# Kernel tuning notes

Hardware: AMD Instinct MI355X
Metric: run time of the kernel (lower is better)

The kernel has to match this reference:

```python
import jax, jax.numpy as jnp
import numpy as np

SCALE_FACTOR = 4.0
DROPOUT_P = 0.5
DROPOUT_KEY = jax.random.key(42)  # fixed key: torch dropout is stochastic; we fix RNG for reproducibility


def setup_inputs() -> dict:
    key = jax.random.key(0)
    k1, k2 = jax.random.split(key)
    x1 = jax.random.normal(k1, (4096, 1024), dtype=jnp.float32)
    x2 = jax.random.normal(k2, (4096, 1024), dtype=jnp.float32)
    return {"x1": x1, "x2": x2}


def reference(x1, x2):
    # scores: [M, N] = x1 @ x2^T, scaled
    scores = jnp.matmul(x1, x2.T) * SCALE_FACTOR
    # F.softmax with no dim on 2-D input -> softmax over dim 1 (keys)
    attn = jax.nn.softmax(scores, axis=-1)
    # dropout p=0.5, train mode (inverted dropout: scale kept units by 1/(1-p))
    keep = jax.random.bernoulli(DROPOUT_KEY, 1.0 - DROPOUT_P, attn.shape)
    attn = jnp.where(keep, attn / (1.0 - DROPOUT_P), 0.0).astype(attn.dtype)
    # output: [M, D] = attn @ x2 (x2 reused as values)
    return jnp.matmul(attn, x2)
```

## Files before the change

### kernel.cpp

```cpp
#include <hip/hip_runtime.h>

typedef unsigned short u16;
typedef unsigned int   u32;
typedef __attribute__((ext_vector_type(4))) float f32x4;
typedef __attribute__((ext_vector_type(8))) short bf16x8;
typedef __attribute__((ext_vector_type(8))) unsigned short u16x8;
typedef __attribute__((ext_vector_type(4))) unsigned short u16x4;

#define MROWS 4096
#define DDIM  1024

__device__ __forceinline__ u16 f2bf(float f) {
  u32 u = __float_as_uint(f);
  return (u16)((u + 0x7FFFu + ((u >> 16) & 1u)) >> 16);
}
__device__ __forceinline__ float bf2f(u16 h) { return __uint_as_float(((u32)h) << 16); }

__global__ __launch_bounds__(256)
void expand3(const float4* __restrict__ x, u16* __restrict__ out, float scale, int patA) {
  int t = blockIdx.x * 256 + threadIdx.x;
  float4 v0 = x[(size_t)t * 2], v1 = x[(size_t)t * 2 + 1];
  float vv[8] = {v0.x*scale, v0.y*scale, v0.z*scale, v0.w*scale,
                 v1.x*scale, v1.y*scale, v1.z*scale, v1.w*scale};
  u16 o[24];
#pragma unroll
  for (int j = 0; j < 8; ++j) {
    u16 h = f2bf(vv[j]);
    u16 l = f2bf(vv[j] - bf2f(h));
    if (patA) { o[3*j]=h; o[3*j+1]=h; o[3*j+2]=l; }
    else      { o[3*j]=h; o[3*j+1]=l; o[3*j+2]=h; }
  }
  u16x8* dst = (u16x8*)(out + (size_t)t * 24);
#pragma unroll
  for (int q = 0; q < 3; ++q) {
    u16x8 w;
#pragma unroll
    for (int j = 0; j < 8; ++j) w[j] = o[q*8+j];
    dst[q] = w;
  }
}

__global__ __launch_bounds__(256)
void transpose_bf16(const float* __restrict__ x2, u16* __restrict__ VT) {
  __shared__ float tile[64][65];
  int tid = threadIdx.x;
  int dt = blockIdx.x;
  int kt = blockIdx.y;
#pragma unroll
  for (int it = 0; it < 16; ++it) {
    int lin = it * 256 + tid;
    int r = lin >> 6, c = lin & 63;
    tile[r][c] = x2[(size_t)(kt*64 + r) * DDIM + dt*64 + c];
  }
  __syncthreads();
#pragma unroll
  for (int it = 0; it < 16; ++it) {
    int lin = it * 256 + tid;
    int dr = lin >> 6, kc = lin & 63;
    VT[(size_t)(dt*64 + dr) * MROWS + kt*64 + kc] = f2bf(tile[kc][dr]);
  }
}

__device__ __forceinline__ void gload16(const u16* g, u16* l) {
  __builtin_amdgcn_global_load_lds(
      (const __attribute__((address_space(1))) void*)g,
      (__attribute__((address_space(3))) void*)l, 16, 0, 0);
}

#define BARRIER() do { asm volatile("" ::: "memory"); __builtin_amdgcn_s_barrier(); \
                       asm volatile("" ::: "memory"); } while (0)
#define LGKM0()   do { asm volatile("s_waitcnt lgkmcnt(0)" ::: "memory"); \
                       __builtin_amdgcn_sched_barrier(0); } while (0)
#define VMCNT6()  do { asm volatile("s_waitcnt vmcnt(6)" ::: "memory"); } while (0)

__device__ __forceinline__ void read_a4(bf16x8 (&aF)[4][2], const u16* base, const int (&off)[4][2]) {
#pragma unroll
  for (int m = 0; m < 4; ++m)
#pragma unroll
    for (int kx = 0; kx < 2; ++kx)
      aF[m][kx] = *(const bf16x8*)(base + off[m][kx]);
}
__device__ __forceinline__ void read_b2(bf16x8 (&bF)[2][2], const u16* base, const int (&off)[2][2]) {
#pragma unroll
  for (int n = 0; n < 2; ++n)
#pragma unroll
    for (int kx = 0; kx < 2; ++kx)
      bF[n][kx] = *(const bf16x8*)(base + off[n][kx]);
}
__device__ __forceinline__ void mma_quad(f32x4 (&acc)[8][4], const bf16x8 (&aF)[4][2],
                                         const bf16x8 (&bF)[2][2], int MH, int NH) {
#pragma unroll
  for (int kx = 0; kx < 2; ++kx)
#pragma unroll
    for (int m = 0; m < 4; ++m)
#pragma unroll
      for (int n = 0; n < 2; ++n)
        acc[MH*4+m][NH*2+n] = __builtin_amdgcn_mfma_f32_16x16x32_bf16(
            aF[m][kx], bF[n][kx], acc[MH*4+m][NH*2+n], 0, 0, 0);
}

__global__ __launch_bounds__(512, 2)
void gemm256(const u16* __restrict__ A, const u16* __restrict__ Bt, float* __restrict__ C,
             int M, int N, int K, int ntpc) {
  __shared__ u16 smem[65536];
  const int tid = threadIdx.x;
  const int lane = tid & 63;
  const int w = tid >> 6;
  const int wr = w >> 2;
  const int wc = w & 3;
  const int fr = lane & 15;
  const int hi = lane >> 4;

  const long bm = (long)blockIdx.y * 256;
  const long bn = (long)blockIdx.x * 256;
  const size_t kcol0 = (size_t)blockIdx.z * ntpc * 64;
  float* Cz = C + (size_t)blockIdx.z * (size_t)M * N;

  const int srow = tid >> 3;
  const int scol = (((tid & 7) ^ (srow & 7)) << 3);
  const u16* Abase = A + (size_t)(bm + srow) * K + kcol0 + scol;
  const u16* Bbase = Bt + (size_t)(bn + srow) * K + kcol0 + scol;

  int offA[4][2], offB[2][2];
#pragma unroll
  for (int m = 0; m < 4; ++m)
#pragma unroll
    for (int kx = 0; kx < 2; ++kx) {
      int r = m*32 + wr*16 + fr;
      int c0 = kx*4 + hi;
      offA[m][kx] = r*64 + (((c0 ^ (r & 7))) << 3);
    }
#pragma unroll
  for (int n = 0; n < 2; ++n)
#pragma unroll
    for (int kx = 0; kx < 2; ++kx) {
      int r = n*64 + wc*16 + fr;
      int c0 = kx*4 + hi;
      offB[n][kx] = r*64 + (((c0 ^ (r & 7))) << 3);
    }

  f32x4 acc[8][4];
#pragma unroll
  for (int m = 0; m < 8; ++m)
#pragma unroll
    for (int n = 0; n < 4; ++n) acc[m][n] = (f32x4){0.f, 0.f, 0.f, 0.f};
  bf16x8 aF[4][2], b0F[2][2], b1F[2][2];

#define STAGE_A(TAU,H,D) do { \
    const u16* _s = Abase + (size_t)(H)*128*K + (size_t)(TAU)*64; \
    u16* _d = smem + ((D)*2+(H))*8192 + tid*8; \
    gload16(_s, _d); gload16(_s + (size_t)64*K, _d + 4096); } while (0)
#define STAGE_B(TAU,H,D) do { \
    const u16* _s = Bbase + (size_t)(H)*128*K + (size_t)(TAU)*64; \
    u16* _d = smem + 32768 + ((D)*2+(H))*8192 + tid*8; \
    gload16(_s, _d); gload16(_s + (size_t)64*K, _d + 4096); } while (0)

  STAGE_A(0,0,0); STAGE_B(0,0,0); STAGE_B(0,1,0); STAGE_A(0,1,0);
  STAGE_A(1,0,1); STAGE_B(1,0,1); STAGE_B(1,1,1);
  VMCNT6();
  BARRIER();

  const int nt = ntpc;
  for (int T = 0; T < nt; T += 2) {
    const int t1 = T + 1;
    const int t2 = (T + 2 < nt) ? T + 2 : nt - 1;
    const int t3 = (T + 3 < nt) ? T + 3 : nt - 1;

    read_a4(aF, smem + 0, offA);
    read_b2(b0F, smem + 32768, offB);
    STAGE_A(t1, 1, 1);
    BARRIER(); LGKM0();
    __builtin_amdgcn_s_setprio(1); mma_quad(acc, aF, b0F, 0, 0); __builtin_amdgcn_s_setprio(0);
    BARRIER();
    read_b2(b1F, smem + 40960, offB);
    STAGE_A(t2, 0, 0);
    BARRIER(); LGKM0();
    __builtin_amdgcn_s_setprio(1); mma_quad(acc, aF, b1F, 0, 1); __builtin_amdgcn_s_setprio(0);
    BARRIER();
    read_a4(aF, smem + 8192, offA);
    STAGE_B(t2, 0, 0);
    BARRIER(); LGKM0();
    __builtin_amdgcn_s_setprio(1); mma_quad(acc, aF, b0F, 1, 0); __builtin_amdgcn_s_setprio(0);
    BARRIER();
    STAGE_B(t2, 1, 0);
    VMCNT6();
    BARRIER(); LGKM0();
    __builtin_amdgcn_s_setprio(1); mma_quad(acc, aF, b1F, 1, 1); __builtin_amdgcn_s_setprio(0);
    BARRIER();
    read_a4(aF, smem + 16384, offA);
    read_b2(b0F, smem + 49152, offB);
    STAGE_A(t2, 1, 0);
    BARRIER(); LGKM0();
    __builtin_amdgcn_s_setprio(1); mma_quad(acc, aF, b0F, 0, 0); __builtin_amdgcn_s_setprio(0);
    BARRIER();
    read_b2(b1F, smem + 57344, offB);
    STAGE_A(t3, 0, 1);
    BARRIER(); LGKM0();
    __builtin_amdgcn_s_setprio(1); mma_quad(acc, aF, b1F, 0, 1); __builtin_amdgcn_s_setprio(0);
    BARRIER();
    read_a4(aF, smem + 24576, offA);
    STAGE_B(t3, 0, 1);
    BARRIER(); LGKM0();
    __builtin_amdgcn_s_setprio(1); mma_quad(acc, aF, b0F, 1, 0); __builtin_amdgcn_s_setprio(0);
    BARRIER();
    STAGE_B(t3, 1, 1);
    VMCNT6();
    BARRIER(); LGKM0();
    __builtin_amdgcn_s_setprio(1); mma_quad(acc, aF, b1F, 1, 1); __builtin_amdgcn_s_setprio(0);
    BARRIER();
  }
#undef STAGE_A
#undef STAGE_B

#pragma unroll
  for (int m = 0; m < 8; ++m)
#pragma unroll
    for (int n = 0; n < 4; ++n) {
      size_t row0 = (size_t)(bm + m*32 + wr*16 + hi*4);
      size_t col  = (size_t)(bn + n*64 + wc*16 + fr);
#pragma unroll
      for (int r = 0; r < 4; ++r)
        Cz[(row0 + r) * N + col] = acc[m][n][r];
    }
}

__device__ __forceinline__ u32 rotl32(u32 x, int r) { return (x << r) | (x >> (32 - r)); }

__device__ __forceinline__ u32 threefry_bits(u32 n) {
  const u32 K0 = 0u, K1 = 42u, K2 = 0x1BD11BDAu ^ 0u ^ 42u;
  u32 x0 = K0;
  u32 x1 = n + K1;
#define TF4(a,b,c,d) \
  x0 += x1; x1 = rotl32(x1, a); x1 ^= x0; \
  x0 += x1; x1 = rotl32(x1, b); x1 ^= x0; \
  x0 += x1; x1 = rotl32(x1, c); x1 ^= x0; \
  x0 += x1; x1 = rotl32(x1, d); x1 ^= x0;
  TF4(13,15,26,6);  x0 += K1; x1 += K2 + 1u;
  TF4(17,29,16,24); x0 += K2; x1 += K0 + 2u;
  TF4(13,15,26,6);  x0 += K0; x1 += K1 + 3u;
  TF4(17,29,16,24); x0 += K1; x1 += K2 + 4u;
  TF4(13,15,26,6);  x0 += K2; x1 += K0 + 5u;
#undef TF4
  return x0 ^ x1;
}

__global__ __launch_bounds__(256)
void softmax_dropout(const float* __restrict__ S, u16* __restrict__ P) {
  const int tid  = threadIdx.x;
  const int lane = tid & 63;
  const int w    = tid >> 6;
  const int row  = blockIdx.x * 4 + w;
  const float4* Sr = (const float4*)(S + (size_t)row * MROWS);
  float4 v[16];
#pragma unroll
  for (int i = 0; i < 16; ++i) v[i] = Sr[i * 64 + lane];
  float m = -3.0e38f;
#pragma unroll
  for (int i = 0; i < 16; ++i)
    m = fmaxf(m, fmaxf(fmaxf(v[i].x, v[i].y), fmaxf(v[i].z, v[i].w)));
#pragma unroll
  for (int off = 32; off > 0; off >>= 1) m = fmaxf(m, __shfl_xor(m, off, 64));
  float s = 0.0f;
#pragma unroll
  for (int i = 0; i < 16; ++i) {
    v[i].x = __expf(v[i].x - m); v[i].y = __expf(v[i].y - m);
    v[i].z = __expf(v[i].z - m); v[i].w = __expf(v[i].w - m);
    s += v[i].x + v[i].y + v[i].z + v[i].w;
  }
#pragma unroll
  for (int off = 32; off > 0; off >>= 1) s += __shfl_xor(s, off, 64);
  const float inv = 2.0f / s;
  u16* Pr = P + (size_t)row * MROWS;
#pragma unroll
  for (int i = 0; i < 16; ++i) {
    int j0 = (i * 64 + lane) * 4;
    u32 base = (u32)row * 4096u + (u32)j0;
    float e[4] = {v[i].x, v[i].y, v[i].z, v[i].w};
    u16x4 o;
#pragma unroll
    for (int c = 0; c < 4; ++c) {
      u32 bits = threefry_bits(base + (u32)c);
      float val = (bits & 0x80000000u) ? 0.0f : e[c] * inv;
      o[c] = f2bf(val);
    }
    *(u16x4*)(Pr + j0) = o;
  }
}

__global__ __launch_bounds__(256)
void reduce4(const float4* __restrict__ p, float4* __restrict__ out) {
  size_t i = (size_t)blockIdx.x * 256 + threadIdx.x;
  const size_t NP = (size_t)MROWS * DDIM / 4;
  float4 a = p[i], b = p[i + NP], c = p[i + 2*NP], d = p[i + 3*NP];
  float4 r;
  r.x = a.x + b.x + c.x + d.x;
  r.y = a.y + b.y + c.y + d.y;
  r.z = a.z + b.z + c.z + d.z;
  r.w = a.w + b.w + c.w + d.w;
  out[i] = r;
}

extern "C" void kernel_launch(void* const* d_in, const int* in_sizes, int n_in,
                              void* d_out, int out_size, void* d_ws, size_t ws_size,
                              hipStream_t stream) {
  const float* x1 = (const float*)d_in[0];
  const float* x2 = (const float*)d_in[1];
  float* out = (float*)d_out;
  char* ws = (char*)d_ws;

  const size_t OFF_XB = 25165824;
  const size_t OFF_VT = 50331648;
  const size_t OFF_S  = 58720256;
  const size_t NEED   = 125829120;
  if (ws_size < NEED) {
    hipMemsetAsync(d_out, 0x7F, (size_t)out_size * sizeof(float), stream);
    return;
  }
  u16*   XA = (u16*)(ws);
  u16*   XB = (u16*)(ws + OFF_XB);
  u16*   VT = (u16*)(ws + OFF_VT);
  float* S  = (float*)(ws + OFF_S);
  float* PT = (float*)(ws + OFF_S);
  u16*   P  = (u16*)(ws);

  expand3<<<2048, 256, 0, stream>>>((const float4*)x1, XA, 4.0f, 1);
  expand3<<<2048, 256, 0, stream>>>((const float4*)x2, XB, 1.0f, 0);
  transpose_bf16<<<dim3(16, 64), 256, 0, stream>>>(x2, VT);
  gemm256<<<dim3(16, 16, 1), 512, 0, stream>>>(XA, XB, S, 4096, 4096, 3072, 48);
  softmax_dropout<<<1024, 256, 0, stream>>>(S, P);
  gemm256<<<dim3(4, 16, 4), 512, 0, stream>>>(P, VT, PT, 4096, 1024, 4096, 16);
  reduce4<<<4096, 256, 0, stream>>>((const float4*)PT, (float4*)out);
}
```

Measured before the change: 199.0 us.

## Precompute dropout bitmask in expand kernels and restructure GEMM LDS reads with block swizzle

Threefry dropout bits move out of softmax into the expand3 kernels, which pack them into a 2 MB bitmask that softmax reads back as words. The GEMM inner loop is reorganised into two 4x4 accumulator halves with even/odd k-fragment reads and grouped staging. A block-index remap spreads neighbouring tiles apart for better cache locality. The intent is to shorten the compute-heavy softmax pass and tighten the GEMM schedule, at the cost of extra mask memory traffic and more work in the expand kernels.

New measurement: 205.5 us. 3.2% more time.

```diff
diff --git a/kernel.cpp b/kernel.cpp
--- a/kernel.cpp
+++ b/kernel.cpp
@@ -16,216 +16,7 @@
 }
 __device__ __forceinline__ float bf2f(u16 h) { return __uint_as_float(((u32)h) << 16); }
 
-__global__ __launch_bounds__(256)
-void expand3(const float4* __restrict__ x, u16* __restrict__ out, float scale, int patA) {
-  int t = blockIdx.x * 256 + threadIdx.x;
-  float4 v0 = x[(size_t)t * 2], v1 = x[(size_t)t * 2 + 1];
-  float vv[8] = {v0.x*scale, v0.y*scale, v0.z*scale, v0.w*scale,
-                 v1.x*scale, v1.y*scale, v1.z*scale, v1.w*scale};
-  u16 o[24];
-#pragma unroll
-  for (int j = 0; j < 8; ++j) {
-    u16 h = f2bf(vv[j]);
-    u16 l = f2bf(vv[j] - bf2f(h));
-    if (patA) { o[3*j]=h; o[3*j+1]=h; o[3*j+2]=l; }
-    else      { o[3*j]=h; o[3*j+1]=l; o[3*j+2]=h; }
-  }
-  u16x8* dst = (u16x8*)(out + (size_t)t * 24);
-#pragma unroll
-  for (int q = 0; q < 3; ++q) {
-    u16x8 w;
-#pragma unroll
-    for (int j = 0; j < 8; ++j) w[j] = o[q*8+j];
-    dst[q] = w;
-  }
-}
-
-__global__ __launch_bounds__(256)
-void transpose_bf16(const float* __restrict__ x2, u16* __restrict__ VT) {
-  __shared__ float tile[64][65];
-  int tid = threadIdx.x;
-  int dt = blockIdx.x;
-  int kt = blockIdx.y;
-#pragma unroll
-  for (int it = 0; it < 16; ++it) {
-    int lin = it * 256 + tid;
-    int r = lin >> 6, c = lin & 63;
-    tile[r][c] = x2[(size_t)(kt*64 + r) * DDIM + dt*64 + c];
-  }
-  __syncthreads();
-#pragma unroll
-  for (int it = 0; it < 16; ++it) {
-    int lin = it * 256 + tid;
-    int dr = lin >> 6, kc = lin & 63;
-    VT[(size_t)(dt*64 + dr) * MROWS + kt*64 + kc] = f2bf(tile[kc][dr]);
-  }
-}
-
-__device__ __forceinline__ void gload16(const u16* g, u16* l) {
-  __builtin_amdgcn_global_load_lds(
-      (const __attribute__((address_space(1))) void*)g,
-      (__attribute__((address_space(3))) void*)l, 16, 0, 0);
-}
-
-#define BARRIER() do { asm volatile("" ::: "memory"); __builtin_amdgcn_s_barrier(); \
-                       asm volatile("" ::: "memory"); } while (0)
-#define LGKM0()   do { asm volatile("s_waitcnt lgkmcnt(0)" ::: "memory"); \
-                       __builtin_amdgcn_sched_barrier(0); } while (0)
-#define VMCNT6()  do { asm volatile("s_waitcnt vmcnt(6)" ::: "memory"); } while (0)
-
-__device__ __forceinline__ void read_a4(bf16x8 (&aF)[4][2], const u16* base, const int (&off)[4][2]) {
-#pragma unroll
-  for (int m = 0; m < 4; ++m)
-#pragma unroll
-    for (int kx = 0; kx < 2; ++kx)
-      aF[m][kx] = *(const bf16x8*)(base + off[m][kx]);
-}
-__device__ __forceinline__ void read_b2(bf16x8 (&bF)[2][2], const u16* base, const int (&off)[2][2]) {
-#pragma unroll
-  for (int n = 0; n < 2; ++n)
-#pragma unroll
-    for (int kx = 0; kx < 2; ++kx)
-      bF[n][kx] = *(const bf16x8*)(base + off[n][kx]);
-}
-__device__ __forceinline__ void mma_quad(f32x4 (&acc)[8][4], const bf16x8 (&aF)[4][2],
-                                         const bf16x8 (&bF)[2][2], int MH, int NH) {
-#pragma unroll
-  for (int kx = 0; kx < 2; ++kx)
-#pragma unroll
-    for (int m = 0; m < 4; ++m)
-#pragma unroll
-      for (int n = 0; n < 2; ++n)
-        acc[MH*4+m][NH*2+n] = __builtin_amdgcn_mfma_f32_16x16x32_bf16(
-            aF[m][kx], bF[n][kx], acc[MH*4+m][NH*2+n], 0, 0, 0);
-}
-
-__global__ __launch_bounds__(512, 2)
-void gemm256(const u16* __restrict__ A, const u16* __restrict__ Bt, float* __restrict__ C,
-             int M, int N, int K, int ntpc) {
-  __shared__ u16 smem[65536];
-  const int tid = threadIdx.x;
-  const int lane = tid & 63;
-  const int w = tid >> 6;
-  const int wr = w >> 2;
-  const int wc = w & 3;
-  const int fr = lane & 15;
-  const int hi = lane >> 4;
-
-  const long bm = (long)blockIdx.y * 256;
-  const long bn = (long)blockIdx.x * 256;
-  const size_t kcol0 = (size_t)blockIdx.z * ntpc * 64;
-  float* Cz = C + (size_t)blockIdx.z * (size_t)M * N;
-
-  const int srow = tid >> 3;
-  const int scol = (((tid & 7) ^ (srow & 7)) << 3);
-  const u16* Abase = A + (size_t)(bm + srow) * K + kcol0 + scol;
-  const u16* Bbase = Bt + (size_t)(bn + srow) * K + kcol0 + scol;
-
-  int offA[4][2], offB[2][2];
-#pragma unroll
-  for (int m = 0; m < 4; ++m)
-#pragma unroll
-    for (int kx = 0; kx < 2; ++kx) {
-      int r = m*32 + wr*16 + fr;
-      int c0 = kx*4 + hi;
-      offA[m][kx] = r*64 + (((c0 ^ (r & 7))) << 3);
-    }
-#pragma unroll
-  for (int n = 0; n < 2; ++n)
-#pragma unroll
-    for (int kx = 0; kx < 2; ++kx) {
-      int r = n*64 + wc*16 + fr;
-      int c0 = kx*4 + hi;
-      offB[n][kx] = r*64 + (((c0 ^ (r & 7))) << 3);
-    }
-
-  f32x4 acc[8][4];
-#pragma unroll
-  for (int m = 0; m < 8; ++m)
-#pragma unroll
-    for (int n = 0; n < 4; ++n) acc[m][n] = (f32x4){0.f, 0.f, 0.f, 0.f};
-  bf16x8 aF[4][2], b0F[2][2], b1F[2][2];
-
-#define STAGE_A(TAU,H,D) do { \
-    const u16* _s = Abase + (size_t)(H)*128*K + (size_t)(TAU)*64; \
-    u16* _d = smem + ((D)*2+(H))*8192 + tid*8; \
-    gload16(_s, _d); gload16(_s + (size_t)64*K, _d + 4096); } while (0)
-#define STAGE_B(TAU,H,D) do { \
-    const u16* _s = Bbase + (size_t)(H)*128*K + (size_t)(TAU)*64; \
-    u16* _d = smem + 32768 + ((D)*2+(H))*8192 + tid*8; \
-    gload16(_s, _d); gload16(_s + (size_t)64*K, _d + 4096); } while (0)
-
-  STAGE_A(0,0,0); STAGE_B(0,0,0); STAGE_B(0,1,0); STAGE_A(0,1,0);
-  STAGE_A(1,0,1); STAGE_B(1,0,1); STAGE_B(1,1,1);
-  VMCNT6();
-  BARRIER();
-
-  const int nt = ntpc;
-  for (int T = 0; T < nt; T += 2) {
-    const int t1 = T + 1;
-    const int t2 = (T + 2 < nt) ? T + 2 : nt - 1;
-    const int t3 = (T + 3 < nt) ? T + 3 : nt - 1;
-
-    read_a4(aF, smem + 0, offA);
-    read_b2(b0F, smem + 32768, offB);
-    STAGE_A(t1, 1, 1);
-    BARRIER(); LGKM0();
-    __builtin_amdgcn_s_setprio(1); mma_quad(acc, aF, b0F, 0, 0); __builtin_amdgcn_s_setprio(0);
-    BARRIER();
-    read_b2(b1F, smem + 40960, offB);
-    STAGE_A(t2, 0, 0);
-    BARRIER(); LGKM0();
-    __builtin_amdgcn_s_setprio(1); mma_quad(acc, aF, b1F, 0, 1); __builtin_amdgcn_s_setprio(0);
-    BARRIER();
-    read_a4(aF, smem + 8192, offA);
-    STAGE_B(t2, 0, 0);
-    BARRIER(); LGKM0();
-    __builtin_amdgcn_s_setprio(1); mma_quad(acc, aF, b0F, 1, 0); __builtin_amdgcn_s_setprio(0);
-    BARRIER();
-    STAGE_B(t2, 1, 0);
-    VMCNT6();
-    BARRIER(); LGKM0();
-    __builtin_amdgcn_s_setprio(1); mma_quad(acc, aF, b1F, 1, 1); __builtin_amdgcn_s_setprio(0);
-    BARRIER();
-    read_a4(aF, smem + 16384, offA);
-    read_b2(b0F, smem + 49152, offB);
-    STAGE_A(t2, 1, 0);
-    BARRIER(); LGKM0();
-    __builtin_amdgcn_s_setprio(1); mma_quad(acc, aF, b0F, 0, 0); __builtin_amdgcn_s_setprio(0);
-    BARRIER();
-    read_b2(b1F, smem + 57344, offB);
-    STAGE_A(t3, 0, 1);
-    BARRIER(); LGKM0();
-    __builtin_amdgcn_s_setprio(1); mma_quad(acc, aF, b1F, 0, 1); __builtin_amdgcn_s_setprio(0);
-    BARRIER();
-    read_a4(aF, smem + 24576, offA);
-    STAGE_B(t3, 0, 1);
-    BARRIER(); LGKM0();
-    __builtin_amdgcn_s_setprio(1); mma_quad(acc, aF, b0F, 1, 0); __builtin_amdgcn_s_setprio(0);
-    BARRIER();
-    STAGE_B(t3, 1, 1);
-    VMCNT6();
-    BARRIER(); LGKM0();
-    __builtin_amdgcn_s_setprio(1); mma_quad(acc, aF, b1F, 1, 1); __builtin_amdgcn_s_setprio(0);
-    BARRIER();
-  }
-#undef STAGE_A
-#undef STAGE_B
-
-#pragma unroll
-  for (int m = 0; m < 8; ++m)
-#pragma unroll
-    for (int n = 0; n < 4; ++n) {
-      size_t row0 = (size_t)(bm + m*32 + wr*16 + hi*4);
-      size_t col  = (size_t)(bn + n*64 + wc*16 + fr);
-#pragma unroll
-      for (int r = 0; r < 4; ++r)
-        Cz[(row0 + r) * N + col] = acc[m][n][r];
-    }
-}
-
 __device__ __forceinline__ u32 rotl32(u32 x, int r) { return (x << r) | (x >> (32 - r)); }
-
 __device__ __forceinline__ u32 threefry_bits(u32 n) {
   const u32 K0 = 0u, K1 = 42u, K2 = 0x1BD11BDAu ^ 0u ^ 42u;
   u32 x0 = K0;
@@ -245,7 +36,223 @@
 }
 
 __global__ __launch_bounds__(256)
-void softmax_dropout(const float* __restrict__ S, u16* __restrict__ P) {
+void expand3(const float4* __restrict__ x, u16* __restrict__ out, float scale, int patA,
+             u32* __restrict__ mask, u32 wordBase, u32 nWords) {
+  int t = blockIdx.x * 256 + threadIdx.x;
+  float4 v0 = x[(size_t)t * 2], v1 = x[(size_t)t * 2 + 1];
+  float vv[8] = {v0.x*scale, v0.y*scale, v0.z*scale, v0.w*scale,
+                 v1.x*scale, v1.y*scale, v1.z*scale, v1.w*scale};
+  u16 o[24];
+#pragma unroll
+  for (int j = 0; j < 8; ++j) {
+    u16 h = f2bf(vv[j]);
+    u16 l = f2bf(vv[j] - bf2f(h));
+    if (patA) { o[3*j]=h; o[3*j+1]=h; o[3*j+2]=l; }
+    else      { o[3*j]=h; o[3*j+1]=l; o[3*j+2]=h; }
+  }
+  u16x8* dst = (u16x8*)(out + (size_t)t * 24);
+#pragma unroll
+  for (int q = 0; q < 3; ++q) {
+    u16x8 wv;
+#pragma unroll
+    for (int j = 0; j < 8; ++j) wv[j] = o[q*8+j];
+    dst[q] = wv;
+  }
+  if ((u32)t < nWords) {
+    u32 wi = wordBase + (u32)t;
+    u32 n0 = wi * 32u;
+    u32 wbits = 0;
+#pragma unroll 4
+    for (int b = 0; b < 32; ++b) wbits |= (threefry_bits(n0 + (u32)b) >> 31) << b;
+    mask[wi] = wbits;
+  }
+}
+
+__global__ __launch_bounds__(256)
+void transpose_bf16(const float* __restrict__ x2, u16* __restrict__ VT) {
+  __shared__ float tile[64][65];
+  int tid = threadIdx.x;
+  int dt = blockIdx.x;
+  int kt = blockIdx.y;
+#pragma unroll
+  for (int it = 0; it < 16; ++it) {
+    int lin = it * 256 + tid;
+    int r = lin >> 6, c = lin & 63;
+    tile[r][c] = x2[(size_t)(kt*64 + r) * DDIM + dt*64 + c];
+  }
+  __syncthreads();
+#pragma unroll
+  for (int it = 0; it < 16; ++it) {
+    int lin = it * 256 + tid;
+    int dr = lin >> 6, kc = lin & 63;
+    VT[(size_t)(dt*64 + dr) * MROWS + kt*64 + kc] = f2bf(tile[kc][dr]);
+  }
+}
+
+__device__ __forceinline__ void gload16(const u16* g, u16* l) {
+  __builtin_amdgcn_global_load_lds(
+      (const __attribute__((address_space(1))) void*)g,
+      (__attribute__((address_space(3))) void*)l, 16, 0, 0);
+}
+
+#define BARRIER() do { asm volatile("" ::: "memory"); __builtin_amdgcn_s_barrier(); \
+                       asm volatile("" ::: "memory"); } while (0)
+#define LGKM0()   do { asm volatile("s_waitcnt lgkmcnt(0)" ::: "memory"); \
+                       __builtin_amdgcn_sched_barrier(0); } while (0)
+#define VMCNT6()  do { asm volatile("s_waitcnt vmcnt(6)" ::: "memory"); } while (0)
+
+__device__ __forceinline__ void mma4x4(f32x4 (&accq)[4][4], const bf16x8 (&a)[4],
+                                       const bf16x8 (&b)[4]) {
+#pragma unroll
+  for (int m = 0; m < 4; ++m)
+#pragma unroll
+    for (int n = 0; n < 4; ++n)
+      accq[m][n] = __builtin_amdgcn_mfma_f32_16x16x32_bf16(a[m], b[n], accq[m][n], 0, 0, 0);
+}
+
+__global__ __launch_bounds__(512, 2)
+void gemm256(const u16* __restrict__ A, const u16* __restrict__ Bt, float* __restrict__ C,
+             int M, int N, int K, int ntpc) {
+  __shared__ u16 smem[65536];
+  const int tid = threadIdx.x;
+  const int lane = tid & 63;
+  const int w = tid >> 6;
+  const int wr = w >> 2;
+  const int wc = w & 3;
+  const int fr = lane & 15;
+  const int hi = lane >> 4;
+
+  const int nbxy = gridDim.x * gridDim.y;
+  const int id0 = blockIdx.y * gridDim.x + blockIdx.x;
+  const int id  = (id0 & 7) * (nbxy >> 3) + (id0 >> 3);
+  const int bxi = id % gridDim.x;
+  const int byi = id / gridDim.x;
+
+  const long bm = (long)byi * 256;
+  const long bn = (long)bxi * 256;
+  const size_t kcol0 = (size_t)blockIdx.z * ntpc * 64;
+  float* Cz = C + (size_t)blockIdx.z * (size_t)M * N;
+
+  const int srow = tid >> 3;
+  const int scol = (((tid & 7) ^ (srow & 7)) << 3);
+  const u16* Abase = A  + (size_t)(bm + srow) * K + kcol0 + scol;
+  const u16* Bbase = Bt + (size_t)(bn + srow) * K + kcol0 + scol;
+
+  const int csw0 = ((hi)     ^ (fr & 7)) << 3;
+  const int csw1 = ((4 + hi) ^ (fr & 7)) << 3;
+  const int arow = (wr*16 + fr) * 64;
+  const int brow = (wc*16 + fr) * 64;
+
+#define RD_A(dst, D, H, CSW) do { \
+    const u16* _b = smem + ((D)*2+(H))*8192 + arow + (CSW); \
+    dst[0] = *(const bf16x8*)(_b); \
+    dst[1] = *(const bf16x8*)(_b + 2048); \
+    dst[2] = *(const bf16x8*)(_b + 4096); \
+    dst[3] = *(const bf16x8*)(_b + 6144); } while (0)
+#define RD_B(dst, D, CSW) do { \
+    const u16* _b0 = smem + 32768 + ((D)*2+0)*8192 + brow + (CSW); \
+    const u16* _b1 = smem + 32768 + ((D)*2+1)*8192 + brow + (CSW); \
+    dst[0] = *(const bf16x8*)(_b0); \
+    dst[1] = *(const bf16x8*)(_b0 + 4096); \
+    dst[2] = *(const bf16x8*)(_b1); \
+    dst[3] = *(const bf16x8*)(_b1 + 4096); } while (0)
+
+  f32x4 accL[4][4], accH[4][4];
+#pragma unroll
+  for (int m = 0; m < 4; ++m)
+#pragma unroll
+    for (int n = 0; n < 4; ++n) {
+      accL[m][n] = (f32x4){0.f, 0.f, 0.f, 0.f};
+      accH[m][n] = (f32x4){0.f, 0.f, 0.f, 0.f};
+    }
+  bf16x8 aE[4], aO[4], bE[4], bO[4];
+
+#define STAGE_A(TAU,H,D) do { \
+    const u16* _s = Abase + (size_t)(H)*128*K + (size_t)(TAU)*64; \
+    u16* _d = smem + ((D)*2+(H))*8192 + tid*8; \
+    gload16(_s, _d); gload16(_s + (size_t)64*K, _d + 4096); } while (0)
+#define STAGE_B(TAU,H,D) do { \
+    const u16* _s = Bbase + (size_t)(H)*128*K + (size_t)(TAU)*64; \
+    u16* _d = smem + 32768 + ((D)*2+(H))*8192 + tid*8; \
+    gload16(_s, _d); gload16(_s + (size_t)64*K, _d + 4096); } while (0)
+
+  STAGE_A(0,0,0); STAGE_B(0,0,0); STAGE_B(0,1,0); STAGE_A(0,1,0);
+  STAGE_A(1,0,1); STAGE_B(1,0,1); STAGE_B(1,1,1);
+  VMCNT6();
+  BARRIER();
+
+  const int nt = ntpc;
+  for (int T = 0; T < nt; T += 2) {
+    const int t1 = T + 1;
+    const int t2 = (T + 2 < nt) ? T + 2 : nt - 1;
+    const int t3 = (T + 3 < nt) ? T + 3 : nt - 1;
+
+    RD_A(aE, 0, 0, csw0);
+    RD_B(bE, 0, csw0);
+    STAGE_A(t1, 1, 1);
+    BARRIER(); LGKM0();
+    __builtin_amdgcn_s_setprio(1); mma4x4(accL, aE, bE); __builtin_amdgcn_s_setprio(0);
+    BARRIER();
+    RD_A(aO, 0, 0, csw1);
+    RD_B(bO, 0, csw1);
+    BARRIER(); LGKM0();
+    __builtin_amdgcn_s_setprio(1); mma4x4(accL, aO, bO); __builtin_amdgcn_s_setprio(0);
+    BARRIER();
+    RD_A(aE, 0, 1, csw0);
+    STAGE_A(t2, 0, 0); STAGE_B(t2, 0, 0); STAGE_B(t2, 1, 0);
+    BARRIER(); LGKM0();
+    __builtin_amdgcn_s_setprio(1); mma4x4(accH, aE, bE); __builtin_amdgcn_s_setprio(0);
+    BARRIER();
+    RD_A(aO, 0, 1, csw1);
+    VMCNT6();
+    BARRIER(); LGKM0();
+    __builtin_amdgcn_s_setprio(1); mma4x4(accH, aO, bO); __builtin_amdgcn_s_setprio(0);
+    BARRIER();
+    RD_A(aE, 1, 0, csw0);
+    RD_B(bE, 1, csw0);
+    STAGE_A(t2, 1, 0);
+    BARRIER(); LGKM0();
+    __builtin_amdgcn_s_setprio(1); mma4x4(accL, aE, bE); __builtin_amdgcn_s_setprio(0);
+    BARRIER();
+    RD_A(aO, 1, 0, csw1);
+    RD_B(bO, 1, csw1);
+    BARRIER(); LGKM0();
+    __builtin_amdgcn_s_setprio(1); mma4x4(accL, aO, bO); __builtin_amdgcn_s_setprio(0);
+    BARRIER();
+    RD_A(aE, 1, 1, csw0);
+    STAGE_A(t3, 0, 1); STAGE_B(t3, 0, 1); STAGE_B(t3, 1, 1);
+    BARRIER(); LGKM0();
+    __builtin_amdgcn_s_setprio(1); mma4x4(accH, aE, bE); __builtin_amdgcn_s_setprio(0);
+    BARRIER();
+    RD_A(aO, 1, 1, csw1);
+    VMCNT6();
+    BARRIER(); LGKM0();
+    __builtin_amdgcn_s_setprio(1); mma4x4(accH, aO, bO); __builtin_amdgcn_s_setprio(0);
+    BARRIER();
+  }
+#undef STAGE_A
+#undef STAGE_B
+#undef RD_A
+#undef RD_B
+
+#pragma unroll
+  for (int m = 0; m < 4; ++m)
+#pragma unroll
+    for (int n = 0; n < 4; ++n) {
+      size_t rowL = (size_t)(bm + m*32 + wr*16 + hi*4);
+      size_t rowH = rowL + 128;
+      size_t col  = (size_t)(bn + n*64 + wc*16 + fr);
+#pragma unroll
+      for (int r = 0; r < 4; ++r) {
+        Cz[(rowL + r) * N + col] = accL[m][n][r];
+        Cz[(rowH + r) * N + col] = accH[m][n][r];
+      }
+    }
+}
+
+__global__ __launch_bounds__(256)
+void softmax_dropout(const float* __restrict__ S, const u32* __restrict__ mask,
+                     u16* __restrict__ P) {
   const int tid  = threadIdx.x;
   const int lane = tid & 63;
   const int w    = tid >> 6;
@@ -271,16 +278,17 @@
   for (int off = 32; off > 0; off >>= 1) s += __shfl_xor(s, off, 64);
   const float inv = 2.0f / s;
   u16* Pr = P + (size_t)row * MROWS;
+  const u32* Mw = mask + (size_t)row * 128;
 #pragma unroll
   for (int i = 0; i < 16; ++i) {
     int j0 = (i * 64 + lane) * 4;
-    u32 base = (u32)row * 4096u + (u32)j0;
+    u32 word = Mw[j0 >> 5];
+    int sh = j0 & 31;
     float e[4] = {v[i].x, v[i].y, v[i].z, v[i].w};
     u16x4 o;
 #pragma unroll
     for (int c = 0; c < 4; ++c) {
-      u32 bits = threefry_bits(base + (u32)c);
-      float val = (bits & 0x80000000u) ? 0.0f : e[c] * inv;
+      float val = ((word >> (sh + c)) & 1u) ? 0.0f : e[c] * inv;
       o[c] = f2bf(val);
     }
     *(u16x4*)(Pr + j0) = o;
@@ -308,10 +316,11 @@
   float* out = (float*)d_out;
   char* ws = (char*)d_ws;
 
-  const size_t OFF_XB = 25165824;
-  const size_t OFF_VT = 50331648;
-  const size_t OFF_S  = 58720256;
-  const size_t NEED   = 125829120;
+  const size_t OFF_XB   = 25165824;
+  const size_t OFF_VT   = 50331648;
+  const size_t OFF_S    = 58720256;
+  const size_t OFF_MASK = 125829120;
+  const size_t NEED     = 127926272;
   if (ws_size < NEED) {
     hipMemsetAsync(d_out, 0x7F, (size_t)out_size * sizeof(float), stream);
     return;
@@ -321,13 +330,14 @@
   u16*   VT = (u16*)(ws + OFF_VT);
   float* S  = (float*)(ws + OFF_S);
   float* PT = (float*)(ws + OFF_S);
+  u32*   MK = (u32*)(ws + OFF_MASK);
   u16*   P  = (u16*)(ws);
 
-  expand3<<<2048, 256, 0, stream>>>((const float4*)x1, XA, 4.0f, 1);
-  expand3<<<2048, 256, 0, stream>>>((const float4*)x2, XB, 1.0f, 0);
+  expand3<<<2048, 256, 0, stream>>>((const float4*)x1, XA, 4.0f, 1, MK, 0u, 262144u);
+  expand3<<<2048, 256, 0, stream>>>((const float4*)x2, XB, 1.0f, 0, MK, 262144u, 262144u);
   transpose_bf16<<<dim3(16, 64), 256, 0, stream>>>(x2, VT);
   gemm256<<<dim3(16, 16, 1), 512, 0, stream>>>(XA, XB, S, 4096, 4096, 3072, 48);
-  softmax_dropout<<<1024, 256, 0, stream>>>(S, P);
+  softmax_dropout<<<1024, 256, 0, stream>>>(S, MK, P);
   gemm256<<<dim3(4, 16, 4), 512, 0, stream>>>(P, VT, PT, 4096, 1024, 4096, 16);
   reduce4<<<4096, 256, 0, stream>>>((const float4*)PT, (float4*)out);
 }
```

## Compute dropout mask bits inside QK^T GEMM mainloop to hide RNG cost

Applied to the files above, without the earlier changes.

The threefry dropout bits are now generated inside the first GEMM's MFMA loop, interleaved between barriers, and packed into a bitmask in workspace. The softmax kernel reads these mask words instead of running threefry per element. The aim is to hide the integer-heavy RNG work under the MFMA-bound GEMM and make softmax memory-bound. The cost is extra VALU work and register pressure in the GEMM plus a small mask write and read.

After: 205.8 us. 1.03x slower.

```diff
diff --git a/kernel.cpp b/kernel.cpp
--- a/kernel.cpp
+++ b/kernel.cpp
@@ -16,216 +16,7 @@
 }
 __device__ __forceinline__ float bf2f(u16 h) { return __uint_as_float(((u32)h) << 16); }
 
-__global__ __launch_bounds__(256)
-void expand3(const float4* __restrict__ x, u16* __restrict__ out, float scale, int patA) {
-  int t = blockIdx.x * 256 + threadIdx.x;
-  float4 v0 = x[(size_t)t * 2], v1 = x[(size_t)t * 2 + 1];
-  float vv[8] = {v0.x*scale, v0.y*scale, v0.z*scale, v0.w*scale,
-                 v1.x*scale, v1.y*scale, v1.z*scale, v1.w*scale};
-  u16 o[24];
-#pragma unroll
-  for (int j = 0; j < 8; ++j) {
-    u16 h = f2bf(vv[j]);
-    u16 l = f2bf(vv[j] - bf2f(h));
-    if (patA) { o[3*j]=h; o[3*j+1]=h; o[3*j+2]=l; }
-    else      { o[3*j]=h; o[3*j+1]=l; o[3*j+2]=h; }
-  }
-  u16x8* dst = (u16x8*)(out + (size_t)t * 24);
-#pragma unroll
-  for (int q = 0; q < 3; ++q) {
-    u16x8 w;
-#pragma unroll
-    for (int j = 0; j < 8; ++j) w[j] = o[q*8+j];
-    dst[q] = w;
-  }
-}
-
-__global__ __launch_bounds__(256)
-void transpose_bf16(const float* __restrict__ x2, u16* __restrict__ VT) {
-  __shared__ float tile[64][65];
-  int tid = threadIdx.x;
-  int dt = blockIdx.x;
-  int kt = blockIdx.y;
-#pragma unroll
-  for (int it = 0; it < 16; ++it) {
-    int lin = it * 256 + tid;
-    int r = lin >> 6, c = lin & 63;
-    tile[r][c] = x2[(size_t)(kt*64 + r) * DDIM + dt*64 + c];
-  }
-  __syncthreads();
-#pragma unroll
-  for (int it = 0; it < 16; ++it) {
-    int lin = it * 256 + tid;
-    int dr = lin >> 6, kc = lin & 63;
-    VT[(size_t)(dt*64 + dr) * MROWS + kt*64 + kc] = f2bf(tile[kc][dr]);
-  }
-}
-
-__device__ __forceinline__ void gload16(const u16* g, u16* l) {
-  __builtin_amdgcn_global_load_lds(
-      (const __attribute__((address_space(1))) void*)g,
-      (__attribute__((address_space(3))) void*)l, 16, 0, 0);
-}
-
-#define BARRIER() do { asm volatile("" ::: "memory"); __builtin_amdgcn_s_barrier(); \
-                       asm volatile("" ::: "memory"); } while (0)
-#define LGKM0()   do { asm volatile("s_waitcnt lgkmcnt(0)" ::: "memory"); \
-                       __builtin_amdgcn_sched_barrier(0); } while (0)
-#define VMCNT6()  do { asm volatile("s_waitcnt vmcnt(6)" ::: "memory"); } while (0)
-
-__device__ __forceinline__ void read_a4(bf16x8 (&aF)[4][2], const u16* base, const int (&off)[4][2]) {
-#pragma unroll
-  for (int m = 0; m < 4; ++m)
-#pragma unroll
-    for (int kx = 0; kx < 2; ++kx)
-      aF[m][kx] = *(const bf16x8*)(base + off[m][kx]);
-}
-__device__ __forceinline__ void read_b2(bf16x8 (&bF)[2][2], const u16* base, const int (&off)[2][2]) {
-#pragma unroll
-  for (int n = 0; n < 2; ++n)
-#pragma unroll
-    for (int kx = 0; kx < 2; ++kx)
-      bF[n][kx] = *(const bf16x8*)(base + off[n][kx]);
-}
-__device__ __forceinline__ void mma_quad(f32x4 (&acc)[8][4], const bf16x8 (&aF)[4][2],
-                                         const bf16x8 (&bF)[2][2], int MH, int NH) {
-#pragma unroll
-  for (int kx = 0; kx < 2; ++kx)
-#pragma unroll
-    for (int m = 0; m < 4; ++m)
-#pragma unroll
-      for (int n = 0; n < 2; ++n)
-        acc[MH*4+m][NH*2+n] = __builtin_amdgcn_mfma_f32_16x16x32_bf16(
-            aF[m][kx], bF[n][kx], acc[MH*4+m][NH*2+n], 0, 0, 0);
-}
-
-__global__ __launch_bounds__(512, 2)
-void gemm256(const u16* __restrict__ A, const u16* __restrict__ Bt, float* __restrict__ C,
-             int M, int N, int K, int ntpc) {
-  __shared__ u16 smem[65536];
-  const int tid = threadIdx.x;
-  const int lane = tid & 63;
-  const int w = tid >> 6;
-  const int wr = w >> 2;
-  const int wc = w & 3;
-  const int fr = lane & 15;
-  const int hi = lane >> 4;
-
-  const long bm = (long)blockIdx.y * 256;
-  const long bn = (long)blockIdx.x * 256;
-  const size_t kcol0 = (size_t)blockIdx.z * ntpc * 64;
-  float* Cz = C + (size_t)blockIdx.z * (size_t)M * N;
-
-  const int srow = tid >> 3;
-  const int scol = (((tid & 7) ^ (srow & 7)) << 3);
-  const u16* Abase = A + (size_t)(bm + srow) * K + kcol0 + scol;
-  const u16* Bbase = Bt + (size_t)(bn + srow) * K + kcol0 + scol;
-
-  int offA[4][2], offB[2][2];
-#pragma unroll
-  for (int m = 0; m < 4; ++m)
-#pragma unroll
-    for (int kx = 0; kx < 2; ++kx) {
-      int r = m*32 + wr*16 + fr;
-      int c0 = kx*4 + hi;
-      offA[m][kx] = r*64 + (((c0 ^ (r & 7))) << 3);
-    }
-#pragma unroll
-  for (int n = 0; n < 2; ++n)
-#pragma unroll
-    for (int kx = 0; kx < 2; ++kx) {
-      int r = n*64 + wc*16 + fr;
-      int c0 = kx*4 + hi;
-      offB[n][kx] = r*64 + (((c0 ^ (r & 7))) << 3);
-    }
-
-  f32x4 acc[8][4];
-#pragma unroll
-  for (int m = 0; m < 8; ++m)
-#pragma unroll
-    for (int n = 0; n < 4; ++n) acc[m][n] = (f32x4){0.f, 0.f, 0.f, 0.f};
-  bf16x8 aF[4][2], b0F[2][2], b1F[2][2];
-
-#define STAGE_A(TAU,H,D) do { \
-    const u16* _s = Abase + (size_t)(H)*128*K + (size_t)(TAU)*64; \
-    u16* _d = smem + ((D)*2+(H))*8192 + tid*8; \
-    gload16(_s, _d); gload16(_s + (size_t)64*K, _d + 4096); } while (0)
-#define STAGE_B(TAU,H,D) do { \
-    const u16* _s = Bbase + (size_t)(H)*128*K + (size_t)(TAU)*64; \
-    u16* _d = smem + 32768 + ((D)*2+(H))*8192 + tid*8; \
-    gload16(_s, _d); gload16(_s + (size_t)64*K, _d + 4096); } while (0)
-
-  STAGE_A(0,0,0); STAGE_B(0,0,0); STAGE_B(0,1,0); STAGE_A(0,1,0);
-  STAGE_A(1,0,1); STAGE_B(1,0,1); STAGE_B(1,1,1);
-  VMCNT6();
-  BARRIER();
-
-  const int nt = ntpc;
-  for (int T = 0; T < nt; T += 2) {
-    const int t1 = T + 1;
-    const int t2 = (T + 2 < nt) ? T + 2 : nt - 1;
-    const int t3 = (T + 3 < nt) ? T + 3 : nt - 1;
-
-    read_a4(aF, smem + 0, offA);
-    read_b2(b0F, smem + 32768, offB);
-    STAGE_A(t1, 1, 1);
-    BARRIER(); LGKM0();
-    __builtin_amdgcn_s_setprio(1); mma_quad(acc, aF, b0F, 0, 0); __builtin_amdgcn_s_setprio(0);
-    BARRIER();
-    read_b2(b1F, smem + 40960, offB);
-    STAGE_A(t2, 0, 0);
-    BARRIER(); LGKM0();
-    __builtin_amdgcn_s_setprio(1); mma_quad(acc, aF, b1F, 0, 1); __builtin_amdgcn_s_setprio(0);
-    BARRIER();
-    read_a4(aF, smem + 8192, offA);
-    STAGE_B(t2, 0, 0);
-    BARRIER(); LGKM0();
-    __builtin_amdgcn_s_setprio(1); mma_quad(acc, aF, b0F, 1, 0); __builtin_amdgcn_s_setprio(0);
-    BARRIER();
-    STAGE_B(t2, 1, 0);
-    VMCNT6();
-    BARRIER(); LGKM0();
-    __builtin_amdgcn_s_setprio(1); mma_quad(acc, aF, b1F, 1, 1); __builtin_amdgcn_s_setprio(0);
-    BARRIER();
-    read_a4(aF, smem + 16384, offA);
-    read_b2(b0F, smem + 49152, offB);
-    STAGE_A(t2, 1, 0);
-    BARRIER(); LGKM0();
-    __builtin_amdgcn_s_setprio(1); mma_quad(acc, aF, b0F, 0, 0); __builtin_amdgcn_s_setprio(0);
-    BARRIER();
-    read_b2(b1F, smem + 57344, offB);
-    STAGE_A(t3, 0, 1);
-    BARRIER(); LGKM0();
-    __builtin_amdgcn_s_setprio(1); mma_quad(acc, aF, b1F, 0, 1); __builtin_amdgcn_s_setprio(0);
-    BARRIER();
-    read_a4(aF, smem + 24576, offA);
-    STAGE_B(t3, 0, 1);
-    BARRIER(); LGKM0();
-    __builtin_amdgcn_s_setprio(1); mma_quad(acc, aF, b0F, 1, 0); __builtin_amdgcn_s_setprio(0);
-    BARRIER();
-    STAGE_B(t3, 1, 1);
-    VMCNT6();
-    BARRIER(); LGKM0();
-    __builtin_amdgcn_s_setprio(1); mma_quad(acc, aF, b1F, 1, 1); __builtin_amdgcn_s_setprio(0);
-    BARRIER();
-  }
-#undef STAGE_A
-#undef STAGE_B
-
-#pragma unroll
-  for (int m = 0; m < 8; ++m)
-#pragma unroll
-    for (int n = 0; n < 4; ++n) {
-      size_t row0 = (size_t)(bm + m*32 + wr*16 + hi*4);
-      size_t col  = (size_t)(bn + n*64 + wc*16 + fr);
-#pragma unroll
-      for (int r = 0; r < 4; ++r)
-        Cz[(row0 + r) * N + col] = acc[m][n][r];
-    }
-}
-
 __device__ __forceinline__ u32 rotl32(u32 x, int r) { return (x << r) | (x >> (32 - r)); }
-
 __device__ __forceinline__ u32 threefry_bits(u32 n) {
   const u32 K0 = 0u, K1 = 42u, K2 = 0x1BD11BDAu ^ 0u ^ 42u;
   u32 x0 = K0;
@@ -245,7 +36,241 @@
 }
 
 __global__ __launch_bounds__(256)
-void softmax_dropout(const float* __restrict__ S, u16* __restrict__ P) {
+void expand3(const float4* __restrict__ x, u16* __restrict__ out, float scale, int patA) {
+  int t = blockIdx.x * 256 + threadIdx.x;
+  float4 v0 = x[(size_t)t * 2], v1 = x[(size_t)t * 2 + 1];
+  float vv[8] = {v0.x*scale, v0.y*scale, v0.z*scale, v0.w*scale,
+                 v1.x*scale, v1.y*scale, v1.z*scale, v1.w*scale};
+  u16 o[24];
+#pragma unroll
+  for (int j = 0; j < 8; ++j) {
+    u16 h = f2bf(vv[j]);
+    u16 l = f2bf(vv[j] - bf2f(h));
+    if (patA) { o[3*j]=h; o[3*j+1]=h; o[3*j+2]=l; }
+    else      { o[3*j]=h; o[3*j+1]=l; o[3*j+2]=h; }
+  }
+  u16x8* dst = (u16x8*)(out + (size_t)t * 24);
+#pragma unroll
+  for (int q = 0; q < 3; ++q) {
+    u16x8 wv;
+#pragma unroll
+    for (int j = 0; j < 8; ++j) wv[j] = o[q*8+j];
+    dst[q] = wv;
+  }
+}
+
+__global__ __launch_bounds__(256)
+void transpose_bf16(const float* __restrict__ x2, u16* __restrict__ VT) {
+  __shared__ float tile[64][65];
+  int tid = threadIdx.x;
+  int dt = blockIdx.x;
+  int kt = blockIdx.y;
+#pragma unroll
+  for (int it = 0; it < 16; ++it) {
+    int lin = it * 256 + tid;
+    int r = lin >> 6, c = lin & 63;
+    tile[r][c] = x2[(size_t)(kt*64 + r) * DDIM + dt*64 + c];
+  }
+  __syncthreads();
+#pragma unroll
+  for (int it = 0; it < 16; ++it) {
+    int lin = it * 256 + tid;
+    int dr = lin >> 6, kc = lin & 63;
+    VT[(size_t)(dt*64 + dr) * MROWS + kt*64 + kc] = f2bf(tile[kc][dr]);
+  }
+}
+
+__device__ __forceinline__ void gload16(const u16* g, u16* l) {
+  __builtin_amdgcn_global_load_lds(
+      (const __attribute__((address_space(1))) void*)g,
+      (__attribute__((address_space(3))) void*)l, 16, 0, 0);
+}
+
+#define BARRIER() do { asm volatile("" ::: "memory"); __builtin_amdgcn_s_barrier(); \
+                       asm volatile("" ::: "memory"); } while (0)
+#define LGKM0()   do { asm volatile("s_waitcnt lgkmcnt(0)" ::: "memory"); \
+                       __builtin_amdgcn_sched_barrier(0); } while (0)
+#define VMCNT6()  do { asm volatile("s_waitcnt vmcnt(6)" ::: "memory"); } while (0)
+
+__device__ __forceinline__ void read_a4(bf16x8 (&aF)[4][2], const u16* base, const int (&off)[4][2]) {
+#pragma unroll
+  for (int m = 0; m < 4; ++m)
+#pragma unroll
+    for (int kx = 0; kx < 2; ++kx)
+      aF[m][kx] = *(const bf16x8*)(base + off[m][kx]);
+}
+__device__ __forceinline__ void read_b2(bf16x8 (&bF)[2][2], const u16* base, const int (&off)[2][2]) {
+#pragma unroll
+  for (int n = 0; n < 2; ++n)
+#pragma unroll
+    for (int kx = 0; kx < 2; ++kx)
+      bF[n][kx] = *(const bf16x8*)(base + off[n][kx]);
+}
+__device__ __forceinline__ void mma_quad(f32x4 (&acc)[8][4], const bf16x8 (&aF)[4][2],
+                                         const bf16x8 (&bF)[2][2], int MH, int NH) {
+#pragma unroll
+  for (int kx = 0; kx < 2; ++kx)
+#pragma unroll
+    for (int m = 0; m < 4; ++m)
+#pragma unroll
+      for (int n = 0; n < 2; ++n)
+        acc[MH*4+m][NH*2+n] = __builtin_amdgcn_mfma_f32_16x16x32_bf16(
+            aF[m][kx], bF[n][kx], acc[MH*4+m][NH*2+n], 0, 0, 0);
+}
+
+template <bool DOMASK>
+__global__ __launch_bounds__(512, 2)
+void gemm256(const u16* __restrict__ A, const u16* __restrict__ Bt, float* __restrict__ C,
+             int M, int N, int K, int ntpc, u32* __restrict__ mask) {
+  __shared__ u16 smem[65536];
+  const int tid = threadIdx.x;
+  const int lane = tid & 63;
+  const int w = tid >> 6;
+  const int wr = w >> 2;
+  const int wc = w & 3;
+  const int fr = lane & 15;
+  const int hi = lane >> 4;
+
+  const long bm = (long)blockIdx.y * 256;
+  const long bn = (long)blockIdx.x * 256;
+  const size_t kcol0 = (size_t)blockIdx.z * ntpc * 64;
+  float* Cz = C + (size_t)blockIdx.z * (size_t)M * N;
+
+  const int srow = tid >> 3;
+  const int scol = (((tid & 7) ^ (srow & 7)) << 3);
+  const u16* Abase = A  + (size_t)(bm + srow) * K + kcol0 + scol;
+  const u16* Bbase = Bt + (size_t)(bn + srow) * K + kcol0 + scol;
+
+  int offA[4][2], offB[2][2];
+#pragma unroll
+  for (int m = 0; m < 4; ++m)
+#pragma unroll
+    for (int kx = 0; kx < 2; ++kx) {
+      int r = m*32 + wr*16 + fr;
+      int c0 = kx*4 + hi;
+      offA[m][kx] = r*64 + (((c0 ^ (r & 7))) << 3);
+    }
+#pragma unroll
+  for (int n = 0; n < 2; ++n)
+#pragma unroll
+    for (int kx = 0; kx < 2; ++kx) {
+      int r = n*64 + wc*16 + fr;
+      int c0 = kx*4 + hi;
+      offB[n][kx] = r*64 + (((c0 ^ (r & 7))) << 3);
+    }
+
+  f32x4 acc[8][4];
+#pragma unroll
+  for (int m = 0; m < 8; ++m)
+#pragma unroll
+    for (int n = 0; n < 4; ++n) acc[m][n] = (f32x4){0.f, 0.f, 0.f, 0.f};
+  bf16x8 aF[4][2], b0F[2][2], b1F[2][2];
+
+  u32 mw0 = 0, mw1 = 0, mw2 = 0, mw3 = 0;
+  u32 ci = 0;
+#define MASK_STEP() do { if (DOMASK) { if (ci < 128u) { \
+    u32 lw  = (u32)tid * 4u + (ci >> 5); \
+    u32 n   = (((u32)bm + (lw >> 3)) << 12) + (u32)bn + ((lw & 7u) << 5) + (ci & 31u); \
+    u32 bit = (threefry_bits(n) >> 31) << (ci & 31u); \
+    u32 sel = ci >> 5; \
+    mw0 |= (sel == 0u) ? bit : 0u; \
+    mw1 |= (sel == 1u) ? bit : 0u; \
+    mw2 |= (sel == 2u) ? bit : 0u; \
+    mw3 |= (sel == 3u) ? bit : 0u; \
+    ++ci; } } } while (0)
+
+#define STAGE_A(TAU,H,D) do { \
+    const u16* _s = Abase + (size_t)(H)*128*K + (size_t)(TAU)*64; \
+    u16* _d = smem + ((D)*2+(H))*8192 + tid*8; \
+    gload16(_s, _d); gload16(_s + (size_t)64*K, _d + 4096); } while (0)
+#define STAGE_B(TAU,H,D) do { \
+    const u16* _s = Bbase + (size_t)(H)*128*K + (size_t)(TAU)*64; \
+    u16* _d = smem + 32768 + ((D)*2+(H))*8192 + tid*8; \
+    gload16(_s, _d); gload16(_s + (size_t)64*K, _d + 4096); } while (0)
+
+  STAGE_A(0,0,0); STAGE_B(0,0,0); STAGE_B(0,1,0); STAGE_A(0,1,0);
+  STAGE_A(1,0,1); STAGE_B(1,0,1); STAGE_B(1,1,1);
+  VMCNT6();
+  BARRIER();
+
+  const int nt = ntpc;
+  for (int T = 0; T < nt; T += 2) {
+    const int t1 = T + 1;
+    const int t2 = (T + 2 < nt) ? T + 2 : nt - 1;
+    const int t3 = (T + 3 < nt) ? T + 3 : nt - 1;
+
+    read_a4(aF, smem + 0, offA);
+    read_b2(b0F, smem + 32768, offB);
+    STAGE_A(t1, 1, 1);
+    BARRIER(); MASK_STEP(); LGKM0();
+    __builtin_amdgcn_s_setprio(1); mma_quad(acc, aF, b0F, 0, 0); __builtin_amdgcn_s_setprio(0);
+    BARRIER();
+    read_b2(b1F, smem + 40960, offB);
+    STAGE_A(t2, 0, 0);
+    BARRIER(); MASK_STEP(); LGKM0();
+    __builtin_amdgcn_s_setprio(1); mma_quad(acc, aF, b1F, 0, 1); __builtin_amdgcn_s_setprio(0);
+    BARRIER();
+    read_a4(aF, smem + 8192, offA);
+    STAGE_B(t2, 0, 0);
+    BARRIER(); MASK_STEP(); LGKM0();
+    __builtin_amdgcn_s_setprio(1); mma_quad(acc, aF, b0F, 1, 0); __builtin_amdgcn_s_setprio(0);
+    BARRIER();
+    STAGE_B(t2, 1, 0);
+    VMCNT6();
+    BARRIER(); MASK_STEP(); LGKM0();
+    __builtin_amdgcn_s_setprio(1); mma_quad(acc, aF, b1F, 1, 1); __builtin_amdgcn_s_setprio(0);
+    BARRIER();
+    read_a4(aF, smem + 16384, offA);
+    read_b2(b0F, smem + 49152, offB);
+    STAGE_A(t2, 1, 0);
+    BARRIER(); MASK_STEP(); LGKM0();
+    __builtin_amdgcn_s_setprio(1); mma_quad(acc, aF, b0F, 0, 0); __builtin_amdgcn_s_setprio(0);
+    BARRIER();
+    read_b2(b1F, smem + 57344, offB);
+    STAGE_A(t3, 0, 1);
+    BARRIER(); MASK_STEP(); LGKM0();
+    __builtin_amdgcn_s_setprio(1); mma_quad(acc, aF, b1F, 0, 1); __builtin_amdgcn_s_setprio(0);
+    BARRIER();
+    read_a4(aF, smem + 24576, offA);
+    STAGE_B(t3, 0, 1);
+    BARRIER(); LGKM0();
+    __builtin_amdgcn_s_setprio(1); mma_quad(acc, aF, b0F, 1, 0); __builtin_amdgcn_s_setprio(0);
+    BARRIER();
+    STAGE_B(t3, 1, 1);
+    VMCNT6();
+    BARRIER(); LGKM0();
+    __builtin_amdgcn_s_setprio(1); mma_quad(acc, aF, b1F, 1, 1); __builtin_amdgcn_s_setprio(0);
+    BARRIER();
+  }
+#undef STAGE_A
+#undef STAGE_B
+#undef MASK_STEP
+
+  if (DOMASK) {
+#pragma unroll
+    for (int j = 0; j < 4; ++j) {
+      u32 lw = (u32)tid * 4u + (u32)j;
+      u32 idx = ((u32)bm + (lw >> 3)) * 128u + ((u32)bn >> 5) + (lw & 7u);
+      u32 val = (j == 0) ? mw0 : (j == 1) ? mw1 : (j == 2) ? mw2 : mw3;
+      mask[idx] = val;
+    }
+  }
+
+#pragma unroll
+  for (int m = 0; m < 8; ++m)
+#pragma unroll
+    for (int n = 0; n < 4; ++n) {
+      size_t row0 = (size_t)(bm + m*32 + wr*16 + hi*4);
+      size_t col  = (size_t)(bn + n*64 + wc*16 + fr);
+#pragma unroll
+      for (int r = 0; r < 4; ++r)
+        Cz[(row0 + r) * N + col] = acc[m][n][r];
+    }
+}
+
+__global__ __launch_bounds__(256)
+void softmax_dropout(const float* __restrict__ S, const u32* __restrict__ mask,
+                     u16* __restrict__ P) {
   const int tid  = threadIdx.x;
   const int lane = tid & 63;
   const int w    = tid >> 6;
@@ -271,16 +296,17 @@
   for (int off = 32; off > 0; off >>= 1) s += __shfl_xor(s, off, 64);
   const float inv = 2.0f / s;
   u16* Pr = P + (size_t)row * MROWS;
+  const u32* Mw = mask + (size_t)row * 128;
 #pragma unroll
   for (int i = 0; i < 16; ++i) {
     int j0 = (i * 64 + lane) * 4;
-    u32 base = (u32)row * 4096u + (u32)j0;
+    u32 word = Mw[j0 >> 5];
+    int sh = j0 & 31;
     float e[4] = {v[i].x, v[i].y, v[i].z, v[i].w};
     u16x4 o;
 #pragma unroll
     for (int c = 0; c < 4; ++c) {
-      u32 bits = threefry_bits(base + (u32)c);
-      float val = (bits & 0x80000000u) ? 0.0f : e[c] * inv;
+      float val = ((word >> (sh + c)) & 1u) ? 0.0f : e[c] * inv;
       o[c] = f2bf(val);
     }
     *(u16x4*)(Pr + j0) = o;
@@ -308,10 +334,11 @@
   float* out = (float*)d_out;
   char* ws = (char*)d_ws;
 
-  const size_t OFF_XB = 25165824;
-  const size_t OFF_VT = 50331648;
-  const size_t OFF_S  = 58720256;
-  const size_t NEED   = 125829120;
+  const size_t OFF_XB   = 25165824;
+  const size_t OFF_VT   = 50331648;
+  const size_t OFF_S    = 58720256;
+  const size_t OFF_MASK = 125829120;
+  const size_t NEED     = 127926272;
   if (ws_size < NEED) {
     hipMemsetAsync(d_out, 0x7F, (size_t)out_size * sizeof(float), stream);
     return;
@@ -321,13 +348,14 @@
   u16*   VT = (u16*)(ws + OFF_VT);
   float* S  = (float*)(ws + OFF_S);
   float* PT = (float*)(ws + OFF_S);
+  u32*   MK = (u32*)(ws + OFF_MASK);
   u16*   P  = (u16*)(ws);
 
   expand3<<<2048, 256, 0, stream>>>((const float4*)x1, XA, 4.0f, 1);
   expand3<<<2048, 256, 0, stream>>>((const float4*)x2, XB, 1.0f, 0);
   transpose_bf16<<<dim3(16, 64), 256, 0, stream>>>(x2, VT);
-  gemm256<<<dim3(16, 16, 1), 512, 0, stream>>>(XA, XB, S, 4096, 4096, 3072, 48);
-  softmax_dropout<<<1024, 256, 0, stream>>>(S, P);
-  gemm256<<<dim3(4, 16, 4), 512, 0, stream>>>(P, VT, PT, 4096, 1024, 4096, 16);
+  gemm256<true><<<dim3(16, 16, 1), 512, 0, stream>>>(XA, XB, S, 4096, 4096, 3072, 48, MK);
+  softmax_dropout<<<1024, 256, 0, stream>>>(S, MK, P);
+  gemm256<false><<<dim3(4, 16, 4), 512, 0, stream>>>(P, VT, PT, 4096, 1024, 4096, 16, nullptr);
   reduce4<<<4096, 256, 0, stream>>>((const float4*)PT, (float4*)out);
 }
```
